# Kernel tuning notes

Hardware: AMD Instinct MI355X
Metric: run time of the kernel (lower is better)

Reference implementation:

```python
import jax, jax.numpy as jnp
import numpy as np

BETA = 0.5   # mean-reversion rate of base drift
EPS = 1e-4   # guards T - t division at the final step


def setup_inputs() -> dict:
    key = jax.random.key(0)
    ks = jax.random.split(key, 8)
    B, DX, DW, H, NS = 1024, 32, 32, 128, 500
    ts = jnp.arange(NS + 1, dtype=jnp.float32) / NS  # uniform grid on [0, 1]
    return {
        "x0": jax.random.normal(ks[0], (B, DX), jnp.float32),
        "ts": ts,
        "dWs": jax.random.normal(ks[1], (NS, B, DW), jnp.float32),
        "W1": jax.random.normal(ks[2], (DX + 1, H), jnp.float32) / np.sqrt(DX + 1),
        "b1": jnp.zeros((H,), jnp.float32),
        "W2": jax.random.normal(ks[3], (H, H), jnp.float32) / np.sqrt(H),
        "b2": jnp.zeros((H,), jnp.float32),
        "W3": jax.random.normal(ks[4], (H, DW), jnp.float32) / np.sqrt(H),
        "b3": jnp.zeros((DW,), jnp.float32),
        "Gmat": 0.3 * jax.random.normal(ks[5], (DX, DW), jnp.float32),
        "mu": jax.random.normal(ks[6], (DX,), jnp.float32),
        "v_target": jax.random.normal(ks[7], (DX,), jnp.float32),
    }


def reference(x0, ts, dWs, W1, b1, W2, b2, W3, b3, Gmat, mu, v_target):
    T = ts[-1]
    dts = jnp.diff(ts)                                   # [NS]
    dW_scaled = dWs * jnp.sqrt(dts)[:, None, None]       # [NS, B, DW]
    a = Gmat @ Gmat.T                                    # diffusion covariance [DX, DX]

    def mlp(t, x):  # x: [B, DX] -> [B, DW]
        inp = jnp.concatenate([jnp.full((x.shape[0], 1), t, x.dtype), x], axis=-1)
        h = jnp.tanh(inp @ W1 + b1)
        h = jnp.tanh(h @ W2 + b2)
        return h @ W3 + b3

    def scan_body(carry, vals):
        t, x, ll = carry
        dt, dW = vals
        r = (v_target - x) / (T - t + EPS)               # guided score r_tilde
        f_base = BETA * (mu - x)
        f_circ = f_base + r @ a                          # a symmetric: a @ r per batch row
        v = mlp(t, x)                                    # nn(t, x)
        drift = f_circ + v @ Gmat.T                      # f + g @ nn_output
        x_new = x + drift * dt + dW @ Gmat.T             # Euler-Maruyama step
        Gval = jnp.einsum('bd,bd->b', f_base, r) - 0.5 * jnp.einsum('bd,bd->b', r, r @ a)
        ll_new = ll + Gval * dt
        return (t + dt, x_new, ll_new), (x_new, v)

    init = (ts[0], x0, jnp.zeros(x0.shape[0], x0.dtype))
    (_, _, ll), (xs, vs) = jax.lax.scan(scan_body, init, (dts, dW_scaled))
    return xs, vs, ll
```

## Files before the change

kernel.cpp:

```cpp
#include <hip/hip_runtime.h>
#include <math.h>

#define NSTEPS 500
#define BATCH  1024
#define DX     32
#define DW     32
#define HDIM   128
#define BETA   0.5f
#define EPSG   1e-4f
#define SC     2.8853900817779268f

typedef short bf8_t __attribute__((ext_vector_type(8)));
typedef float f4_t  __attribute__((ext_vector_type(4)));

union U8 { bf8_t v; unsigned u[4]; };

__device__ __forceinline__ f4_t MFMA(bf8_t a, bf8_t b, f4_t c) {
    return __builtin_amdgcn_mfma_f32_16x16x32_bf16(a, b, c, 0, 0, 0);
}

__device__ __forceinline__ unsigned short f2bf(float x) {
    unsigned u = __float_as_uint(x);
    u += 0x7fffu + ((u >> 16) & 1u);
    return (unsigned short)(u >> 16);
}
__device__ __forceinline__ float bf2f(unsigned short h) {
    return __uint_as_float(((unsigned)h) << 16);
}
__device__ __forceinline__ unsigned cvtpk(float a, float b) {
    unsigned r;
    asm("v_cvt_pk_bf16_f32 %0, %1, %2" : "=v"(r) : "v"(a), "v"(b));
    return r;
}
__device__ __forceinline__ float unplo(unsigned u) { return __uint_as_float(u << 16); }
__device__ __forceinline__ float unphi(unsigned u) { return __uint_as_float(u & 0xffff0000u); }

__device__ __forceinline__ float exp2_hw(float x) {
    float r; asm("v_exp_f32 %0, %1" : "=v"(r) : "v"(x)); return r;
}
__device__ __forceinline__ float rcp_hw(float x) {
    float r; asm("v_rcp_f32 %0, %1" : "=v"(r) : "v"(x)); return r;
}
__device__ __forceinline__ float sigm_s(float zs) {
    return rcp_hw(exp2_hw(zs) + 1.f);
}
__device__ __forceinline__ void hilo_pk(float a, float b, unsigned& hp, unsigned& lp) {
    hp = cvtpk(a, b);
    lp = cvtpk(a - unplo(hp), b - unphi(hp));
}
__device__ __forceinline__ void agpr_pin(bf8_t& v) { asm("" : "+a"(v)); }

__device__ __forceinline__ void bar_lds() {
    __builtin_amdgcn_sched_barrier(0);
    asm volatile("s_waitcnt lgkmcnt(0)" ::: "memory");
    __builtin_amdgcn_s_barrier();
    __builtin_amdgcn_sched_barrier(0);
}

__global__ __launch_bounds__(128, 1)
void sde_kernel(const float* __restrict__ x0, const float* __restrict__ ts,
                const float* __restrict__ dWs,
                const float* __restrict__ W1, const float* __restrict__ b1,
                const float* __restrict__ W2, const float* __restrict__ b2,
                const float* __restrict__ W3, const float* __restrict__ b3,
                const float* __restrict__ G,  const float* __restrict__ mu,
                const float* __restrict__ vt, float* __restrict__ out)
{
    __shared__ float sts[NSTEPS + 1];
    __shared__ __align__(16) float sG[DX * DW];
    __shared__ __align__(16) unsigned sXB[2][64][2];
    __shared__ __align__(16) unsigned sRH[2][64][2];
    __shared__ __align__(16) unsigned sRL[2][64][2];
    __shared__ __align__(16) unsigned sBH[4][64][4];
    __shared__ __align__(16) unsigned sB2[4][64][4];
    __shared__ __align__(16) unsigned sUH[2][64][2];
    __shared__ __align__(16) unsigned sUL[2][64][2];
    __shared__ float sLL[2][16];

    const int tid  = threadIdx.x;
    const int w    = tid >> 6;
    const int ow   = 1 - w;
    const int lane = tid & 63;
    const int m16  = lane & 15;
    const int quad = lane >> 4;
    const int r0   = blockIdx.x * 16;
    const int brow = r0 + m16;

    for (int i = tid; i <= NSTEPS; i += 128) sts[i] = ts[i];
    for (int i = tid; i < DX * DW; i += 128) sG[i] = G[i];
    __syncthreads();

    int foS[8], foW[8], ktG[4];
    #pragma unroll
    for (int j = 0; j < 8; ++j) {
        foS[j] = (j < 4) ? (4 * quad + j) : (16 + 4 * quad + (j - 4));
        foW[j] = ((j < 4) ? w * 16 : ow * 16) + 4 * quad + (j & 3);
    }
    ktG[0] = 2 * w; ktG[1] = 2 * w + 1; ktG[2] = 2 * ow; ktG[3] = 2 * ow + 1;

    bf8_t w1a[4];
    #pragma unroll
    for (int ml = 0; ml < 4; ++ml) {
        int mtg = 4 * w + ml;
        #pragma unroll
        for (int j = 0; j < 8; ++j)
            w1a[ml][j] = (short)f2bf(SC * W1[(1 + foW[j]) * HDIM + mtg * 16 + m16]);
        agpr_pin(w1a[ml]);
    }
    bf8_t w2a[4][4];
    #pragma unroll
    for (int ml = 0; ml < 4; ++ml) {
        int mtg = 4 * w + ml;
        #pragma unroll
        for (int kf = 0; kf < 4; ++kf) {
            #pragma unroll
            for (int j = 0; j < 8; ++j)
                w2a[ml][kf][j] = (short)f2bf(-2.f * SC * W2[(ktG[kf] * 32 + foS[j]) * HDIM + mtg * 16 + m16]);
            agpr_pin(w2a[ml][kf]);
        }
    }
    bf8_t w3a[4];
    #pragma unroll
    for (int kf = 0; kf < 4; ++kf) {
        #pragma unroll
        for (int j = 0; j < 8; ++j)
            w3a[kf][j] = (short)f2bf(-2.f * W3[(ktG[kf] * 32 + foS[j]) * DW + w * 16 + m16]);
        agpr_pin(w3a[kf]);
    }

    bf8_t ones;
    #pragma unroll
    for (int j = 0; j < 8; ++j) ones[j] = (short)0x3f80;

    f4_t b2C[4];
    #pragma unroll
    for (int ml = 0; ml < 4; ++ml) {
        f4_t S = {0, 0, 0, 0};
        #pragma unroll
        for (int kf = 0; kf < 4; ++kf) S = MFMA(w2a[ml][kf], ones, S);
        #pragma unroll
        for (int i = 0; i < 4; ++i)
            b2C[ml][i] = fmaf(-0.5f, S[i], SC * b2[(4 * w + ml) * 16 + 4 * quad + i]);
    }
    f4_t b3C;
    {
        f4_t S = {0, 0, 0, 0};
        #pragma unroll
        for (int kf = 0; kf < 4; ++kf) S = MFMA(w3a[kf], ones, S);
        #pragma unroll
        for (int i = 0; i < 4; ++i)
            b3C[i] = fmaf(-0.5f, S[i], b3[w * 16 + 4 * quad + i]);
    }

    f4_t cin[4];
    unsigned w10p[8];
    {
        float t0 = ts[0];
        #pragma unroll
        for (int ml = 0; ml < 4; ++ml) {
            int f0 = (4 * w + ml) * 16 + 4 * quad;
            float wa = SC * W1[f0],     wb = SC * W1[f0 + 1];
            float wc = SC * W1[f0 + 2], wd = SC * W1[f0 + 3];
            w10p[2 * ml]     = ((unsigned)f2bf(wb) << 16) | f2bf(wa);
            w10p[2 * ml + 1] = ((unsigned)f2bf(wd) << 16) | f2bf(wc);
            cin[ml][0] = fmaf(t0, wa, SC * b1[f0]);
            cin[ml][1] = fmaf(t0, wb, SC * b1[f0 + 1]);
            cin[ml][2] = fmaf(t0, wc, SC * b1[f0 + 2]);
            cin[ml][3] = fmaf(t0, wd, SC * b1[f0 + 3]);
        }
    }

    f4_t bmu;
    float vtr[4];
    #pragma unroll
    for (int i = 0; i < 4; ++i) {
        int f = w * 16 + 4 * quad + i;
        bmu[i] = BETA * mu[f];
        vtr[i] = vt[f];
    }

    bf8_t ahi, alo, ghi, glo;
    {
        int rowA = w * 16 + m16;
        float gb[32];
        const f4_t* pb = (const f4_t*)(sG + rowA * DW);
        #pragma unroll
        for (int k4 = 0; k4 < 8; ++k4) {
            f4_t t = pb[k4];
            gb[4 * k4] = t[0]; gb[4 * k4 + 1] = t[1]; gb[4 * k4 + 2] = t[2]; gb[4 * k4 + 3] = t[3];
        }
        #pragma unroll
        for (int j = 0; j < 8; ++j) {
            const f4_t* pa = (const f4_t*)(sG + foW[j] * DW);
            float acc = 0.f;
            #pragma unroll
            for (int k4 = 0; k4 < 8; ++k4) {
                f4_t t = pa[k4];
                acc += t[0] * gb[4 * k4] + t[1] * gb[4 * k4 + 1]
                     + t[2] * gb[4 * k4 + 2] + t[3] * gb[4 * k4 + 3];
            }
            unsigned short h = f2bf(acc);
            ahi[j] = (short)h;
            alo[j] = (short)f2bf(acc - bf2f(h));
            float gv = sG[rowA * DW + foW[j]];
            unsigned short hg = f2bf(gv);
            ghi[j] = (short)hg;
            glo[j] = (short)f2bf(gv - bf2f(hg));
        }
    }

    f4_t xr = ((const f4_t*)(x0 + (size_t)brow * DX))[w * 4 + quad];
    f4_t cw = ((const f4_t*)(dWs + (size_t)brow * DW))[w * 4 + quad];

    const float T = sts[NSTEPS];
    float tcur = sts[0];
    float llr = 0.f;

    float* xs_out = out;
    float* vs_out = out + (size_t)NSTEPS * BATCH * DX;
    float* ll_out = out + (size_t)2 * NSTEPS * BATCH * DX;

    #pragma unroll 1
    for (int s = 0; s < NSTEPS; ++s) {
        const float tnx    = sts[s + 1];
        const float dt     = tnx - tcur;
        const float sqdt   = __builtin_amdgcn_sqrtf(dt);
        const float invrem = rcp_hw(T - tcur + EPSG);

        f4_t nw;
        {
            int sn = (s + 1 < NSTEPS) ? s + 1 : s;
            nw = ((const f4_t*)(dWs + (size_t)sn * (BATCH * DW) + (size_t)brow * DW))[w * 4 + quad];
        }

        float rr[4];
        #pragma unroll
        for (int i = 0; i < 4; ++i) rr[i] = (vtr[i] - xr[i]) * invrem;
        unsigned rh0, rh1, rl0, rl1;
        hilo_pk(rr[0], rr[1], rh0, rl0);
        hilo_pk(rr[2], rr[3], rh1, rl1);
        unsigned xb0 = cvtpk(xr[0], xr[1]), xb1 = cvtpk(xr[2], xr[3]);
        *(uint2*)&sXB[w][lane][0] = make_uint2(xb0, xb1);
        *(uint2*)&sRH[w][lane][0] = make_uint2(rh0, rh1);
        *(uint2*)&sRL[w][lane][0] = make_uint2(rl0, rl1);
        bar_lds();
        uint2 pxb = *(const uint2*)&sXB[ow][lane][0];
        uint2 prh = *(const uint2*)&sRH[ow][lane][0];
        uint2 prl = *(const uint2*)&sRL[ow][lane][0];
        U8 xbF, rhF, rlF;
        xbF.u[0] = xb0; xbF.u[1] = xb1; xbF.u[2] = pxb.x; xbF.u[3] = pxb.y;
        rhF.u[0] = rh0; rhF.u[1] = rh1; rhF.u[2] = prh.x; rhF.u[3] = prh.y;
        rlF.u[0] = rl0; rlF.u[1] = rl1; rlF.u[2] = prl.x; rlF.u[3] = prl.y;

        U8 bhO[2];
        #pragma unroll
        for (int ml = 0; ml < 4; ++ml) {
            f4_t acc = MFMA(w1a[ml], xbF.v, cin[ml]);
            bhO[ml >> 1].u[(2 * ml) & 3]     = cvtpk(sigm_s(acc[0]), sigm_s(acc[1]));
            bhO[ml >> 1].u[(2 * ml + 1) & 3] = cvtpk(sigm_s(acc[2]), sigm_s(acc[3]));
        }
        f4_t ra = {0, 0, 0, 0};
        ra = MFMA(ahi, rhF.v, ra);
        ra = MFMA(ahi, rlF.v, ra);
        ra = MFMA(alo, rhF.v, ra);

        *(uint4*)&sBH[2 * w][lane][0]     = make_uint4(bhO[0].u[0], bhO[0].u[1], bhO[0].u[2], bhO[0].u[3]);
        *(uint4*)&sBH[2 * w + 1][lane][0] = make_uint4(bhO[1].u[0], bhO[1].u[1], bhO[1].u[2], bhO[1].u[3]);
        bar_lds();
        U8 bhF2, bhF3;
        {
            uint4 t2 = *(const uint4*)&sBH[2 * ow][lane][0];
            uint4 t3 = *(const uint4*)&sBH[2 * ow + 1][lane][0];
            bhF2.u[0] = t2.x; bhF2.u[1] = t2.y; bhF2.u[2] = t2.z; bhF2.u[3] = t2.w;
            bhF3.u[0] = t3.x; bhF3.u[1] = t3.y; bhF3.u[2] = t3.z; bhF3.u[3] = t3.w;
        }

        U8 b2O[2];
        #pragma unroll
        for (int ml = 0; ml < 4; ++ml) {
            f4_t acc = b2C[ml];
            acc = MFMA(w2a[ml][0], bhO[0].v, acc);
            acc = MFMA(w2a[ml][1], bhO[1].v, acc);
            acc = MFMA(w2a[ml][2], bhF2.v, acc);
            acc = MFMA(w2a[ml][3], bhF3.v, acc);
            b2O[ml >> 1].u[(2 * ml) & 3]     = cvtpk(sigm_s(acc[0]), sigm_s(acc[1]));
            b2O[ml >> 1].u[(2 * ml + 1) & 3] = cvtpk(sigm_s(acc[2]), sigm_s(acc[3]));
        }
        *(uint4*)&sB2[2 * w][lane][0]     = make_uint4(b2O[0].u[0], b2O[0].u[1], b2O[0].u[2], b2O[0].u[3]);
        *(uint4*)&sB2[2 * w + 1][lane][0] = make_uint4(b2O[1].u[0], b2O[1].u[1], b2O[1].u[2], b2O[1].u[3]);
        bar_lds();
        U8 b2F2, b2F3;
        {
            uint4 t2 = *(const uint4*)&sB2[2 * ow][lane][0];
            uint4 t3 = *(const uint4*)&sB2[2 * ow + 1][lane][0];
            b2F2.u[0] = t2.x; b2F2.u[1] = t2.y; b2F2.u[2] = t2.z; b2F2.u[3] = t2.w;
            b2F3.u[0] = t3.x; b2F3.u[1] = t3.y; b2F3.u[2] = t3.z; b2F3.u[3] = t3.w;
        }

        f4_t vA = b3C;
        vA = MFMA(w3a[0], b2O[0].v, vA);
        vA = MFMA(w3a[1], b2O[1].v, vA);
        vA = MFMA(w3a[2], b2F2.v, vA);
        vA = MFMA(w3a[3], b2F3.v, vA);

        float u_[4];
        #pragma unroll
        for (int i = 0; i < 4; ++i) u_[i] = fmaf(vA[i], dt, cw[i] * sqdt);
        unsigned uh0, uh1, ul0, ul1;
        hilo_pk(u_[0], u_[1], uh0, ul0);
        hilo_pk(u_[2], u_[3], uh1, ul1);
        *(uint2*)&sUH[w][lane][0] = make_uint2(uh0, uh1);
        *(uint2*)&sUL[w][lane][0] = make_uint2(ul0, ul1);
        bar_lds();
        uint2 puh = *(const uint2*)&sUH[ow][lane][0];
        uint2 pul = *(const uint2*)&sUL[ow][lane][0];
        U8 uhF, ulF;
        uhF.u[0] = uh0; uhF.u[1] = uh1; uhF.u[2] = puh.x; uhF.u[3] = puh.y;
        ulF.u[0] = ul0; ulF.u[1] = ul1; ulF.u[2] = pul.x; ulF.u[3] = pul.y;

        f4_t xg = {0, 0, 0, 0};
        xg = MFMA(ghi, uhF.v, xg);
        xg = MFMA(ghi, ulF.v, xg);
        xg = MFMA(glo, uhF.v, xg);

        float gs = 0.f;
        f4_t xo;
        #pragma unroll
        for (int i = 0; i < 4; ++i) {
            float fb = fmaf(-BETA, xr[i], bmu[i]);
            gs = fmaf(fb, rr[i], gs);
            gs = fmaf(-0.5f * rr[i], ra[i], gs);
            float xn = fmaf(fb + ra[i], dt, xr[i]) + xg[i];
            xr[i] = xn;
            xo[i] = xn;
        }
        llr = fmaf(gs, dt, llr);
        ((f4_t*)(xs_out + (size_t)s * (BATCH * DX) + (size_t)brow * DX))[w * 4 + quad] = xo;
        ((f4_t*)(vs_out + (size_t)s * (BATCH * DX) + (size_t)brow * DX))[w * 4 + quad] = vA;

        #pragma unroll
        for (int ml = 0; ml < 4; ++ml) {
            unsigned wa = w10p[2 * ml], wb = w10p[2 * ml + 1];
            cin[ml][0] = fmaf(dt, unplo(wa), cin[ml][0]);
            cin[ml][1] = fmaf(dt, unphi(wa), cin[ml][1]);
            cin[ml][2] = fmaf(dt, unplo(wb), cin[ml][2]);
            cin[ml][3] = fmaf(dt, unphi(wb), cin[ml][3]);
        }
        cw = nw;
        tcur = tnx;
    }

    llr += __shfl_xor(llr, 16, 64);
    llr += __shfl_xor(llr, 32, 64);
    if (lane < 16) sLL[w][lane] = llr;
    bar_lds();
    if (w == 0 && lane < 16) ll_out[r0 + lane] = sLL[0][lane] + sLL[1][lane];
}

extern "C" void kernel_launch(void* const* d_in, const int* in_sizes, int n_in,
                              void* d_out, int out_size, void* d_ws, size_t ws_size,
                              hipStream_t stream) {
    const float* x0 = (const float*)d_in[0];
    const float* ts = (const float*)d_in[1];
    const float* dWs = (const float*)d_in[2];
    const float* W1 = (const float*)d_in[3];
    const float* b1 = (const float*)d_in[4];
    const float* W2 = (const float*)d_in[5];
    const float* b2 = (const float*)d_in[6];
    const float* W3 = (const float*)d_in[7];
    const float* b3 = (const float*)d_in[8];
    const float* G  = (const float*)d_in[9];
    const float* mu = (const float*)d_in[10];
    const float* vt = (const float*)d_in[11];
    hipLaunchKernelGGL(sde_kernel, dim3(BATCH / 16), dim3(128), 0, stream,
                       x0, ts, dWs, W1, b1, W2, b2, W3, b3, G, mu, vt, (float*)d_out);
}
```

Baseline: 857.0 us.

## Split per-step SDE work across four waves with specialized output and score roles

Each block now runs four wavefronts instead of two. The hidden-layer MFMAs are split four ways, so each wave owns 32 hidden units and keeps fewer weight fragments. Waves 0-1 compute the final layer and the noise increment, while waves 2-3 compute the guided-score term r·a and the log-likelihood in parallel. The x update is done redundantly by every wave. The aim is to shorten the serial per-step critical path of this latency-bound scan, at the cost of more LDS exchanges and three block-wide barriers per step across four waves.

```diff
diff --git a/kernel.cpp b/kernel.cpp
--- a/kernel.cpp
+++ b/kernel.cpp
@@ -57,7 +57,7 @@
     __builtin_amdgcn_sched_barrier(0);
 }
 
-__global__ __launch_bounds__(128, 1)
+__global__ __launch_bounds__(256, 1)
 void sde_kernel(const float* __restrict__ x0, const float* __restrict__ ts,
                 const float* __restrict__ dWs,
                 const float* __restrict__ W1, const float* __restrict__ b1,
@@ -68,49 +68,44 @@
 {
     __shared__ float sts[NSTEPS + 1];
     __shared__ __align__(16) float sG[DX * DW];
-    __shared__ __align__(16) unsigned sXB[2][64][2];
-    __shared__ __align__(16) unsigned sRH[2][64][2];
-    __shared__ __align__(16) unsigned sRL[2][64][2];
-    __shared__ __align__(16) unsigned sBH[4][64][4];
+    __shared__ __align__(16) unsigned sH1[4][64][4];
     __shared__ __align__(16) unsigned sB2[4][64][4];
     __shared__ __align__(16) unsigned sUH[2][64][2];
     __shared__ __align__(16) unsigned sUL[2][64][2];
+    __shared__ __align__(16) f4_t sRA[2][64];
     __shared__ float sLL[2][16];
 
     const int tid  = threadIdx.x;
     const int w    = tid >> 6;
-    const int ow   = 1 - w;
     const int lane = tid & 63;
     const int m16  = lane & 15;
     const int quad = lane >> 4;
     const int r0   = blockIdx.x * 16;
     const int brow = r0 + m16;
 
-    for (int i = tid; i <= NSTEPS; i += 128) sts[i] = ts[i];
-    for (int i = tid; i < DX * DW; i += 128) sG[i] = G[i];
+    for (int i = tid; i <= NSTEPS; i += 256) sts[i] = ts[i];
+    for (int i = tid; i < DX * DW; i += 256) sG[i] = G[i];
     __syncthreads();
 
-    int foS[8], foW[8], ktG[4];
-    #pragma unroll
-    for (int j = 0; j < 8; ++j) {
-        foS[j] = (j < 4) ? (4 * quad + j) : (16 + 4 * quad + (j - 4));
-        foW[j] = ((j < 4) ? w * 16 : ow * 16) + 4 * quad + (j & 3);
-    }
-    ktG[0] = 2 * w; ktG[1] = 2 * w + 1; ktG[2] = 2 * ow; ktG[3] = 2 * ow + 1;
-
-    bf8_t w1a[4];
-    #pragma unroll
-    for (int ml = 0; ml < 4; ++ml) {
-        int mtg = 4 * w + ml;
+    int foS[8], ktG[4];
+    #pragma unroll
+    for (int j = 0; j < 8; ++j) foS[j] = (j < 4) ? (4 * quad + j) : (16 + 4 * quad + (j - 4));
+    #pragma unroll
+    for (int kf = 0; kf < 4; ++kf) ktG[kf] = (w + kf) & 3;
+
+    bf8_t w1a[2];
+    #pragma unroll
+    for (int ml = 0; ml < 2; ++ml) {
+        int mtg = 2 * w + ml;
         #pragma unroll
         for (int j = 0; j < 8; ++j)
-            w1a[ml][j] = (short)f2bf(SC * W1[(1 + foW[j]) * HDIM + mtg * 16 + m16]);
+            w1a[ml][j] = (short)f2bf(SC * W1[(1 + foS[j]) * HDIM + mtg * 16 + m16]);
         agpr_pin(w1a[ml]);
     }
-    bf8_t w2a[4][4];
-    #pragma unroll
-    for (int ml = 0; ml < 4; ++ml) {
-        int mtg = 4 * w + ml;
+    bf8_t w2a[2][4];
+    #pragma unroll
+    for (int ml = 0; ml < 2; ++ml) {
+        int mtg = 2 * w + ml;
         #pragma unroll
         for (int kf = 0; kf < 4; ++kf) {
             #pragma unroll
@@ -119,46 +114,29 @@
             agpr_pin(w2a[ml][kf]);
         }
     }
-    bf8_t w3a[4];
-    #pragma unroll
-    for (int kf = 0; kf < 4; ++kf) {
-        #pragma unroll
-        for (int j = 0; j < 8; ++j)
-            w3a[kf][j] = (short)f2bf(-2.f * W3[(ktG[kf] * 32 + foS[j]) * DW + w * 16 + m16]);
-        agpr_pin(w3a[kf]);
-    }
 
     bf8_t ones;
     #pragma unroll
     for (int j = 0; j < 8; ++j) ones[j] = (short)0x3f80;
 
-    f4_t b2C[4];
-    #pragma unroll
-    for (int ml = 0; ml < 4; ++ml) {
+    f4_t b2C[2];
+    #pragma unroll
+    for (int ml = 0; ml < 2; ++ml) {
         f4_t S = {0, 0, 0, 0};
         #pragma unroll
         for (int kf = 0; kf < 4; ++kf) S = MFMA(w2a[ml][kf], ones, S);
         #pragma unroll
         for (int i = 0; i < 4; ++i)
-            b2C[ml][i] = fmaf(-0.5f, S[i], SC * b2[(4 * w + ml) * 16 + 4 * quad + i]);
-    }
-    f4_t b3C;
-    {
-        f4_t S = {0, 0, 0, 0};
-        #pragma unroll
-        for (int kf = 0; kf < 4; ++kf) S = MFMA(w3a[kf], ones, S);
-        #pragma unroll
-        for (int i = 0; i < 4; ++i)
-            b3C[i] = fmaf(-0.5f, S[i], b3[w * 16 + 4 * quad + i]);
-    }
-
-    f4_t cin[4];
-    unsigned w10p[8];
+            b2C[ml][i] = fmaf(-0.5f, S[i], SC * b2[(2 * w + ml) * 16 + 4 * quad + i]);
+    }
+
+    f4_t cin[2];
+    unsigned w10p[4];
     {
         float t0 = ts[0];
         #pragma unroll
-        for (int ml = 0; ml < 4; ++ml) {
-            int f0 = (4 * w + ml) * 16 + 4 * quad;
+        for (int ml = 0; ml < 2; ++ml) {
+            int f0 = (2 * w + ml) * 16 + 4 * quad;
             float wa = SC * W1[f0],     wb = SC * W1[f0 + 1];
             float wc = SC * W1[f0 + 2], wd = SC * W1[f0 + 3];
             w10p[2 * ml]     = ((unsigned)f2bf(wb) << 16) | f2bf(wa);
@@ -170,18 +148,49 @@
         }
     }
 
-    f4_t bmu;
-    float vtr[4];
-    #pragma unroll
-    for (int i = 0; i < 4; ++i) {
-        int f = w * 16 + 4 * quad + i;
-        bmu[i] = BETA * mu[f];
-        vtr[i] = vt[f];
-    }
-
-    bf8_t ahi, alo, ghi, glo;
-    {
-        int rowA = w * 16 + m16;
+    f4_t bmu[2];
+    float vtr[2][4];
+    #pragma unroll
+    for (int mt = 0; mt < 2; ++mt)
+        #pragma unroll
+        for (int i = 0; i < 4; ++i) {
+            int f = mt * 16 + 4 * quad + i;
+            bmu[mt][i] = BETA * mu[f];
+            vtr[mt][i] = vt[f];
+        }
+
+    bf8_t ghi[2], glo[2];
+    #pragma unroll
+    for (int mt = 0; mt < 2; ++mt) {
+        #pragma unroll
+        for (int j = 0; j < 8; ++j) {
+            float gv = sG[(mt * 16 + m16) * DW + foS[j]];
+            unsigned short hg = f2bf(gv);
+            ghi[mt][j] = (short)hg;
+            glo[mt][j] = (short)f2bf(gv - bf2f(hg));
+        }
+        agpr_pin(ghi[mt]); agpr_pin(glo[mt]);
+    }
+
+    bf8_t w3a[4], ahi, alo;
+    f4_t b3C, cw;
+    if (w < 2) {
+        #pragma unroll
+        for (int kf = 0; kf < 4; ++kf) {
+            #pragma unroll
+            for (int j = 0; j < 8; ++j)
+                w3a[kf][j] = (short)f2bf(-2.f * W3[(ktG[kf] * 32 + foS[j]) * DW + w * 16 + m16]);
+            agpr_pin(w3a[kf]);
+        }
+        f4_t S = {0, 0, 0, 0};
+        #pragma unroll
+        for (int kf = 0; kf < 4; ++kf) S = MFMA(w3a[kf], ones, S);
+        #pragma unroll
+        for (int i = 0; i < 4; ++i)
+            b3C[i] = fmaf(-0.5f, S[i], b3[w * 16 + 4 * quad + i]);
+        cw = ((const f4_t*)(dWs + (size_t)brow * DW))[w * 4 + quad];
+    } else {
+        int rowA = (w - 2) * 16 + m16;
         float gb[32];
         const f4_t* pb = (const f4_t*)(sG + rowA * DW);
         #pragma unroll
@@ -191,7 +200,7 @@
         }
         #pragma unroll
         for (int j = 0; j < 8; ++j) {
-            const f4_t* pa = (const f4_t*)(sG + foW[j] * DW);
+            const f4_t* pa = (const f4_t*)(sG + foS[j] * DW);
             float acc = 0.f;
             #pragma unroll
             for (int k4 = 0; k4 < 8; ++k4) {
@@ -202,15 +211,15 @@
             unsigned short h = f2bf(acc);
             ahi[j] = (short)h;
             alo[j] = (short)f2bf(acc - bf2f(h));
-            float gv = sG[rowA * DW + foW[j]];
-            unsigned short hg = f2bf(gv);
-            ghi[j] = (short)hg;
-            glo[j] = (short)f2bf(gv - bf2f(hg));
-        }
-    }
-
-    f4_t xr = ((const f4_t*)(x0 + (size_t)brow * DX))[w * 4 + quad];
-    f4_t cw = ((const f4_t*)(dWs + (size_t)brow * DW))[w * 4 + quad];
+        }
+        agpr_pin(ahi); agpr_pin(alo);
+    }
+
+    f4_t xr[2];
+    {
+        const f4_t* p = (const f4_t*)(x0 + (size_t)brow * DX);
+        xr[0] = p[quad]; xr[1] = p[4 + quad];
+    }
 
     const float T = sts[NSTEPS];
     float tcur = sts[0];
@@ -228,131 +237,147 @@
         const float invrem = rcp_hw(T - tcur + EPSG);
 
         f4_t nw;
-        {
+        if (w < 2) {
             int sn = (s + 1 < NSTEPS) ? s + 1 : s;
             nw = ((const f4_t*)(dWs + (size_t)sn * (BATCH * DW) + (size_t)brow * DW))[w * 4 + quad];
         }
 
-        float rr[4];
-        #pragma unroll
-        for (int i = 0; i < 4; ++i) rr[i] = (vtr[i] - xr[i]) * invrem;
-        unsigned rh0, rh1, rl0, rl1;
-        hilo_pk(rr[0], rr[1], rh0, rl0);
-        hilo_pk(rr[2], rr[3], rh1, rl1);
-        unsigned xb0 = cvtpk(xr[0], xr[1]), xb1 = cvtpk(xr[2], xr[3]);
-        *(uint2*)&sXB[w][lane][0] = make_uint2(xb0, xb1);
-        *(uint2*)&sRH[w][lane][0] = make_uint2(rh0, rh1);
-        *(uint2*)&sRL[w][lane][0] = make_uint2(rl0, rl1);
+        U8 xb;
+        xb.u[0] = cvtpk(xr[0][0], xr[0][1]); xb.u[1] = cvtpk(xr[0][2], xr[0][3]);
+        xb.u[2] = cvtpk(xr[1][0], xr[1][1]); xb.u[3] = cvtpk(xr[1][2], xr[1][3]);
+        U8 bhO;
+        #pragma unroll
+        for (int ml = 0; ml < 2; ++ml) {
+            f4_t acc = MFMA(w1a[ml], xb.v, cin[ml]);
+            bhO.u[2 * ml]     = cvtpk(sigm_s(acc[0]), sigm_s(acc[1]));
+            bhO.u[2 * ml + 1] = cvtpk(sigm_s(acc[2]), sigm_s(acc[3]));
+        }
+        *(uint4*)&sH1[w][lane][0] = make_uint4(bhO.u[0], bhO.u[1], bhO.u[2], bhO.u[3]);
+
+        float rr[2][4];
+        f4_t raO;
+        if (w >= 2) {
+            #pragma unroll
+            for (int mt = 0; mt < 2; ++mt)
+                #pragma unroll
+                for (int i = 0; i < 4; ++i) rr[mt][i] = (vtr[mt][i] - xr[mt][i]) * invrem;
+            U8 rh, rl;
+            hilo_pk(rr[0][0], rr[0][1], rh.u[0], rl.u[0]);
+            hilo_pk(rr[0][2], rr[0][3], rh.u[1], rl.u[1]);
+            hilo_pk(rr[1][0], rr[1][1], rh.u[2], rl.u[2]);
+            hilo_pk(rr[1][2], rr[1][3], rh.u[3], rl.u[3]);
+            raO = f4_t{0, 0, 0, 0};
+            raO = MFMA(ahi, rh.v, raO);
+            raO = MFMA(ahi, rl.v, raO);
+            raO = MFMA(alo, rh.v, raO);
+        }
         bar_lds();
-        uint2 pxb = *(const uint2*)&sXB[ow][lane][0];
-        uint2 prh = *(const uint2*)&sRH[ow][lane][0];
-        uint2 prl = *(const uint2*)&sRL[ow][lane][0];
-        U8 xbF, rhF, rlF;
-        xbF.u[0] = xb0; xbF.u[1] = xb1; xbF.u[2] = pxb.x; xbF.u[3] = pxb.y;
-        rhF.u[0] = rh0; rhF.u[1] = rh1; rhF.u[2] = prh.x; rhF.u[3] = prh.y;
-        rlF.u[0] = rl0; rlF.u[1] = rl1; rlF.u[2] = prl.x; rlF.u[3] = prl.y;
-
-        U8 bhO[2];
-        #pragma unroll
-        for (int ml = 0; ml < 4; ++ml) {
-            f4_t acc = MFMA(w1a[ml], xbF.v, cin[ml]);
-            bhO[ml >> 1].u[(2 * ml) & 3]     = cvtpk(sigm_s(acc[0]), sigm_s(acc[1]));
-            bhO[ml >> 1].u[(2 * ml + 1) & 3] = cvtpk(sigm_s(acc[2]), sigm_s(acc[3]));
-        }
-        f4_t ra = {0, 0, 0, 0};
-        ra = MFMA(ahi, rhF.v, ra);
-        ra = MFMA(ahi, rlF.v, ra);
-        ra = MFMA(alo, rhF.v, ra);
-
-        *(uint4*)&sBH[2 * w][lane][0]     = make_uint4(bhO[0].u[0], bhO[0].u[1], bhO[0].u[2], bhO[0].u[3]);
-        *(uint4*)&sBH[2 * w + 1][lane][0] = make_uint4(bhO[1].u[0], bhO[1].u[1], bhO[1].u[2], bhO[1].u[3]);
+
+        uint4 h1 = *(const uint4*)&sH1[ktG[1]][lane][0];
+        uint4 h2 = *(const uint4*)&sH1[ktG[2]][lane][0];
+        uint4 h3 = *(const uint4*)&sH1[ktG[3]][lane][0];
+        U8 f1, f2, f3;
+        f1.u[0] = h1.x; f1.u[1] = h1.y; f1.u[2] = h1.z; f1.u[3] = h1.w;
+        f2.u[0] = h2.x; f2.u[1] = h2.y; f2.u[2] = h2.z; f2.u[3] = h2.w;
+        f3.u[0] = h3.x; f3.u[1] = h3.y; f3.u[2] = h3.z; f3.u[3] = h3.w;
+        U8 b2O;
+        #pragma unroll
+        for (int ml = 0; ml < 2; ++ml) {
+            f4_t acc = b2C[ml];
+            acc = MFMA(w2a[ml][0], bhO.v, acc);
+            acc = MFMA(w2a[ml][1], f1.v, acc);
+            acc = MFMA(w2a[ml][2], f2.v, acc);
+            acc = MFMA(w2a[ml][3], f3.v, acc);
+            b2O.u[2 * ml]     = cvtpk(sigm_s(acc[0]), sigm_s(acc[1]));
+            b2O.u[2 * ml + 1] = cvtpk(sigm_s(acc[2]), sigm_s(acc[3]));
+        }
+        *(uint4*)&sB2[w][lane][0] = make_uint4(b2O.u[0], b2O.u[1], b2O.u[2], b2O.u[3]);
         bar_lds();
-        U8 bhF2, bhF3;
-        {
-            uint4 t2 = *(const uint4*)&sBH[2 * ow][lane][0];
-            uint4 t3 = *(const uint4*)&sBH[2 * ow + 1][lane][0];
-            bhF2.u[0] = t2.x; bhF2.u[1] = t2.y; bhF2.u[2] = t2.z; bhF2.u[3] = t2.w;
-            bhF3.u[0] = t3.x; bhF3.u[1] = t3.y; bhF3.u[2] = t3.z; bhF3.u[3] = t3.w;
-        }
-
-        U8 b2O[2];
-        #pragma unroll
-        for (int ml = 0; ml < 4; ++ml) {
-            f4_t acc = b2C[ml];
-            acc = MFMA(w2a[ml][0], bhO[0].v, acc);
-            acc = MFMA(w2a[ml][1], bhO[1].v, acc);
-            acc = MFMA(w2a[ml][2], bhF2.v, acc);
-            acc = MFMA(w2a[ml][3], bhF3.v, acc);
-            b2O[ml >> 1].u[(2 * ml) & 3]     = cvtpk(sigm_s(acc[0]), sigm_s(acc[1]));
-            b2O[ml >> 1].u[(2 * ml + 1) & 3] = cvtpk(sigm_s(acc[2]), sigm_s(acc[3]));
-        }
-        *(uint4*)&sB2[2 * w][lane][0]     = make_uint4(b2O[0].u[0], b2O[0].u[1], b2O[0].u[2], b2O[0].u[3]);
-        *(uint4*)&sB2[2 * w + 1][lane][0] = make_uint4(b2O[1].u[0], b2O[1].u[1], b2O[1].u[2], b2O[1].u[3]);
+
+        f4_t vA;
+        if (w < 2) {
+            uint4 p1 = *(const uint4*)&sB2[ktG[1]][lane][0];
+            uint4 p2 = *(const uint4*)&sB2[ktG[2]][lane][0];
+            uint4 p3 = *(const uint4*)&sB2[ktG[3]][lane][0];
+            U8 g1, g2, g3;
+            g1.u[0] = p1.x; g1.u[1] = p1.y; g1.u[2] = p1.z; g1.u[3] = p1.w;
+            g2.u[0] = p2.x; g2.u[1] = p2.y; g2.u[2] = p2.z; g2.u[3] = p2.w;
+            g3.u[0] = p3.x; g3.u[1] = p3.y; g3.u[2] = p3.z; g3.u[3] = p3.w;
+            vA = b3C;
+            vA = MFMA(w3a[0], b2O.v, vA);
+            vA = MFMA(w3a[1], g1.v, vA);
+            vA = MFMA(w3a[2], g2.v, vA);
+            vA = MFMA(w3a[3], g3.v, vA);
+            float u0 = fmaf(vA[0], dt, cw[0] * sqdt);
+            float u1 = fmaf(vA[1], dt, cw[1] * sqdt);
+            float u2 = fmaf(vA[2], dt, cw[2] * sqdt);
+            float u3 = fmaf(vA[3], dt, cw[3] * sqdt);
+            unsigned uh0, uh1, ul0, ul1;
+            hilo_pk(u0, u1, uh0, ul0);
+            hilo_pk(u2, u3, uh1, ul1);
+            *(uint2*)&sUH[w][lane][0] = make_uint2(uh0, uh1);
+            *(uint2*)&sUL[w][lane][0] = make_uint2(ul0, ul1);
+        } else {
+            sRA[w - 2][lane] = raO;
+            int tw = w - 2;
+            float gs = 0.f;
+            #pragma unroll
+            for (int i = 0; i < 4; ++i) {
+                float fb = fmaf(-BETA, xr[tw][i], bmu[tw][i]);
+                gs = fmaf(fb, rr[tw][i], gs);
+                gs = fmaf(-0.5f * rr[tw][i], raO[i], gs);
+            }
+            llr = fmaf(gs, dt, llr);
+        }
         bar_lds();
-        U8 b2F2, b2F3;
-        {
-            uint4 t2 = *(const uint4*)&sB2[2 * ow][lane][0];
-            uint4 t3 = *(const uint4*)&sB2[2 * ow + 1][lane][0];
-            b2F2.u[0] = t2.x; b2F2.u[1] = t2.y; b2F2.u[2] = t2.z; b2F2.u[3] = t2.w;
-            b2F3.u[0] = t3.x; b2F3.u[1] = t3.y; b2F3.u[2] = t3.z; b2F3.u[3] = t3.w;
-        }
-
-        f4_t vA = b3C;
-        vA = MFMA(w3a[0], b2O[0].v, vA);
-        vA = MFMA(w3a[1], b2O[1].v, vA);
-        vA = MFMA(w3a[2], b2F2.v, vA);
-        vA = MFMA(w3a[3], b2F3.v, vA);
-
-        float u_[4];
-        #pragma unroll
-        for (int i = 0; i < 4; ++i) u_[i] = fmaf(vA[i], dt, cw[i] * sqdt);
-        unsigned uh0, uh1, ul0, ul1;
-        hilo_pk(u_[0], u_[1], uh0, ul0);
-        hilo_pk(u_[2], u_[3], uh1, ul1);
-        *(uint2*)&sUH[w][lane][0] = make_uint2(uh0, uh1);
-        *(uint2*)&sUL[w][lane][0] = make_uint2(ul0, ul1);
-        bar_lds();
-        uint2 puh = *(const uint2*)&sUH[ow][lane][0];
-        uint2 pul = *(const uint2*)&sUL[ow][lane][0];
+
+        uint2 ua = *(const uint2*)&sUH[0][lane][0];
+        uint2 ub = *(const uint2*)&sUH[1][lane][0];
+        uint2 la = *(const uint2*)&sUL[0][lane][0];
+        uint2 lb = *(const uint2*)&sUL[1][lane][0];
         U8 uhF, ulF;
-        uhF.u[0] = uh0; uhF.u[1] = uh1; uhF.u[2] = puh.x; uhF.u[3] = puh.y;
-        ulF.u[0] = ul0; ulF.u[1] = ul1; ulF.u[2] = pul.x; ulF.u[3] = pul.y;
-
-        f4_t xg = {0, 0, 0, 0};
-        xg = MFMA(ghi, uhF.v, xg);
-        xg = MFMA(ghi, ulF.v, xg);
-        xg = MFMA(glo, uhF.v, xg);
-
-        float gs = 0.f;
-        f4_t xo;
+        uhF.u[0] = ua.x; uhF.u[1] = ua.y; uhF.u[2] = ub.x; uhF.u[3] = ub.y;
+        ulF.u[0] = la.x; ulF.u[1] = la.y; ulF.u[2] = lb.x; ulF.u[3] = lb.y;
+        f4_t raF0 = sRA[0][lane];
+        f4_t raF1 = sRA[1][lane];
+        f4_t xg0 = {0, 0, 0, 0}, xg1 = {0, 0, 0, 0};
+        xg0 = MFMA(ghi[0], uhF.v, xg0);
+        xg0 = MFMA(ghi[0], ulF.v, xg0);
+        xg0 = MFMA(glo[0], uhF.v, xg0);
+        xg1 = MFMA(ghi[1], uhF.v, xg1);
+        xg1 = MFMA(ghi[1], ulF.v, xg1);
+        xg1 = MFMA(glo[1], uhF.v, xg1);
+        f4_t xo0, xo1;
         #pragma unroll
         for (int i = 0; i < 4; ++i) {
-            float fb = fmaf(-BETA, xr[i], bmu[i]);
-            gs = fmaf(fb, rr[i], gs);
-            gs = fmaf(-0.5f * rr[i], ra[i], gs);
-            float xn = fmaf(fb + ra[i], dt, xr[i]) + xg[i];
-            xr[i] = xn;
-            xo[i] = xn;
-        }
-        llr = fmaf(gs, dt, llr);
-        ((f4_t*)(xs_out + (size_t)s * (BATCH * DX) + (size_t)brow * DX))[w * 4 + quad] = xo;
-        ((f4_t*)(vs_out + (size_t)s * (BATCH * DX) + (size_t)brow * DX))[w * 4 + quad] = vA;
-
-        #pragma unroll
-        for (int ml = 0; ml < 4; ++ml) {
+            float fb0 = fmaf(-BETA, xr[0][i], bmu[0][i]);
+            float fb1 = fmaf(-BETA, xr[1][i], bmu[1][i]);
+            xo0[i] = fmaf(fb0 + raF0[i], dt, xr[0][i]) + xg0[i];
+            xo1[i] = fmaf(fb1 + raF1[i], dt, xr[1][i]) + xg1[i];
+        }
+        xr[0] = xo0; xr[1] = xo1;
+        if (w < 2) {
+            ((f4_t*)(xs_out + (size_t)s * (BATCH * DX) + (size_t)brow * DX))[w * 4 + quad] = (w == 0) ? xo0 : xo1;
+            ((f4_t*)(vs_out + (size_t)s * (BATCH * DX) + (size_t)brow * DX))[w * 4 + quad] = vA;
+            cw = nw;
+        }
+
+        #pragma unroll
+        for (int ml = 0; ml < 2; ++ml) {
             unsigned wa = w10p[2 * ml], wb = w10p[2 * ml + 1];
             cin[ml][0] = fmaf(dt, unplo(wa), cin[ml][0]);
             cin[ml][1] = fmaf(dt, unphi(wa), cin[ml][1]);
             cin[ml][2] = fmaf(dt, unplo(wb), cin[ml][2]);
             cin[ml][3] = fmaf(dt, unphi(wb), cin[ml][3]);
         }
-        cw = nw;
         tcur = tnx;
     }
 
-    llr += __shfl_xor(llr, 16, 64);
-    llr += __shfl_xor(llr, 32, 64);
-    if (lane < 16) sLL[w][lane] = llr;
+    if (w >= 2) {
+        llr += __shfl_xor(llr, 16, 64);
+        llr += __shfl_xor(llr, 32, 64);
+        if (lane < 16) sLL[w - 2][lane] = llr;
+    }
     bar_lds();
     if (w == 0 && lane < 16) ll_out[r0 + lane] = sLL[0][lane] + sLL[1][lane];
 }
@@ -372,6 +397,6 @@
     const float* G  = (const float*)d_in[9];
     const float* mu = (const float*)d_in[10];
     const float* vt = (const float*)d_in[11];
-    hipLaunchKernelGGL(sde_kernel, dim3(BATCH / 16), dim3(128), 0, stream,
+    hipLaunchKernelGGL(sde_kernel, dim3(BATCH / 16), dim3(256), 0, stream,
                        x0, ts, dWs, W1, b1, W2, b2, W3, b3, G, mu, vt, (float*)d_out);
 }
```

Result: faster. 816.2 us (-4.8%).
